# Kernel tuning notes

Hardware: AMD Instinct MI355X
Metric: run time of the kernel (lower is better)

Reference implementation:

```python
import jax, jax.numpy as jnp
import numpy as np

H_RENDER = 640   # hard-coded render resolution in the torch forward
W_RENDER = 640
OUT_H = 128      # self.height
OUT_W = 128      # self.width
NUM_VERTS = 778  # MANO hand mesh
NUM_FACES = 1538
BATCH = 4
BG_DEPTH = 1e10  # z-buffer background, clamped to 100 afterwards


def setup_inputs() -> dict:
    key = jax.random.key(0)
    k1, k2, k3 = jax.random.split(key, 3)
    # screen-space x,y in [0, 640), positive depth z
    xy = jax.random.uniform(k1, (BATCH, NUM_VERTS, 2), minval=0.0, maxval=640.0)
    z = jax.random.uniform(k2, (BATCH, NUM_VERTS, 1), minval=0.3, maxval=1.5)
    vertices = jnp.concatenate([xy, z], axis=-1).astype(jnp.float32)
    faces = jax.random.randint(k3, (NUM_FACES, 3), 0, NUM_VERTS)
    # right_hand=True: swap face columns 0 and 1 (winding flip), as in __init__
    faces = faces[:, jnp.array([1, 0, 2])].astype(jnp.int64)
    return {"vertices": vertices, "faces": faces}


def _edge(ax, ay, bx, by, px, py):
    # signed area of (a, b, p); standard rasterizer edge function
    return (bx - ax) * (py - ay) - (by - ay) * (px - ax)


def _rasterize(face_vertices):
    # face_vertices: [B, F, 3(vertex), 3(x,y,z)] -> z-buffer depth map [B, H, W]
    B = face_vertices.shape[0]
    ys, xs = jnp.meshgrid(
        jnp.arange(H_RENDER, dtype=jnp.float32) + 0.5,
        jnp.arange(W_RENDER, dtype=jnp.float32) + 0.5,
        indexing='ij',
    )  # pixel centers, [H, W]

    def step(zbuf, tri):
        # tri: [B, 3, 3] -> per-vertex coords broadcast to [B, 1, 1]
        x = tri[:, :, 0][:, :, None, None]
        y = tri[:, :, 1][:, :, None, None]
        z = tri[:, :, 2][:, :, None, None]
        x0, x1, x2 = x[:, 0], x[:, 1], x[:, 2]
        y0, y1, y2 = y[:, 0], y[:, 1], y[:, 2]
        z0, z1, z2 = z[:, 0], z[:, 1], z[:, 2]
        e0 = _edge(x1, y1, x2, y2, xs, ys)  # weight of v0
        e1 = _edge(x2, y2, x0, y0, xs, ys)  # weight of v1
        e2 = _edge(x0, y0, x1, y1, xs, ys)  # weight of v2
        area = _edge(x0, y0, x1, y1, x2, y2)  # [B,1,1]
        s = jnp.sign(area)
        valid = jnp.abs(area) > 1e-12
        inside = (e0 * s >= 0) & (e1 * s >= 0) & (e2 * s >= 0) & valid
        safe_area = jnp.where(valid, area, 1.0)
        zpix = (e0 * z0 + e1 * z1 + e2 * z2) / safe_area  # barycentric depth
        cand = jnp.where(inside, zpix, jnp.float32(BG_DEPTH))
        return jnp.minimum(zbuf, cand), None

    zbuf0 = jnp.full((B, H_RENDER, W_RENDER), BG_DEPTH, dtype=jnp.float32)
    zbuf, _ = jax.lax.scan(step, zbuf0, jnp.swapaxes(face_vertices, 0, 1))
    return zbuf


def reference(vertices, faces):
    B = vertices.shape[0]
    F = faces.shape[0]
    # vertex gather: vertices[:, faces.view(-1), 0:3].view(B, F, 3, 3)
    fv = vertices[:, faces.reshape(-1), 0:3].reshape(B, F, 3, 3)
    dm = _rasterize(fv)
    dm = jnp.minimum(dm, 100.0)  # torch.clamp(max=100.0)
    # bilinear resize, align_corners=False (half-pixel), no antialias, like F.interpolate
    resized = jax.image.resize(dm[:, None], (B, 1, OUT_H, OUT_W), method='linear', antialias=False)
    return resized[:, 0]
```

## Files before the change

### kernel.cpp

```cpp
#include <hip/hip_runtime.h>


#pragma clang fp contract(off)

#define H_OUT 128
#define W_OUT 128
#define NV 778
#define NF 1538
#define NB 4
#define NCHUNK 25
#define NFP (NCHUNK * 64)
#define BG100 0x42C80000u


__global__ __launch_bounds__(256) void prep_kernel(
    const float* __restrict__ verts,
    const int* __restrict__ faces,
    float* __restrict__ bbox,
    float* __restrict__ data,
    unsigned int* __restrict__ outu)
{
    int t = blockIdx.x * 256 + threadIdx.x;
    outu[t] = BG100;
    if (t >= NB * NFP) return;
    int b = t / NFP;
    int f = t - b * NFP;
    float* bb = bbox + (size_t)t * 4;
    if (f >= NF) {
        bb[0] = 1e30f; bb[1] = -1e30f; bb[2] = 1e30f; bb[3] = -1e30f;
        return;
    }
    int i0 = faces[f * 3 + 0];
    int i1 = faces[f * 3 + 1];
    int i2 = faces[f * 3 + 2];
    const float* vb = verts + (size_t)b * NV * 3;
    float x0 = vb[i0 * 3 + 0], y0 = vb[i0 * 3 + 1], z0 = vb[i0 * 3 + 2];
    float x1 = vb[i1 * 3 + 0], y1 = vb[i1 * 3 + 1], z1 = vb[i1 * 3 + 2];
    float x2 = vb[i2 * 3 + 0], y2 = vb[i2 * 3 + 1], z2 = vb[i2 * 3 + 2];

    float dx12 = x2 - x1, dy12 = y2 - y1;
    float dx02 = x0 - x2, dy02 = y0 - y2;
    float dx01 = x1 - x0, dy01 = y1 - y0;
    float y20 = y2 - y0, x20 = x2 - x0;
    float area = dx01 * y20 - dy01 * x20;

    float s = 0.0f;
    if (fabsf(area) > 1e-12f) s = (area > 0.0f) ? 1.0f : -1.0f;

    float xmin = fminf(fminf(x0, x1), x2), xmax = fmaxf(fmaxf(x0, x1), x2);
    float ymin = fminf(fminf(y0, y1), y2), ymax = fmaxf(fmaxf(y0, y1), y2);
    if (s == 0.0f) { xmin = 1e30f; xmax = -1e30f; }

    bb[0] = xmin; bb[1] = xmax; bb[2] = ymin; bb[3] = ymax;

    float* o = data + (size_t)t * 16;
    o[0] = s * dx12; o[1] = s * dy12;
    o[2] = s * dx02; o[3] = s * dy02;
    o[4] = s * dx01; o[5] = s * dy01;
    o[6] = x0;  o[7] = y0;  o[8] = x1;  o[9] = y1;  o[10] = x2; o[11] = y2;
    o[12] = z0; o[13] = z1; o[14] = z2; o[15] = s * area;
}

__global__ __launch_bounds__(128) void raster_kernel(
    const float* __restrict__ bbox,
    const float* __restrict__ data,
    unsigned int* __restrict__ outu)
{
    __shared__ float lds[64 * 16];

    int blk = blockIdx.x;
    int tile  = blk & 127;
    int b     = (blk >> 7) & 3;
    int chunk = blk >> 9;
    int tid = threadIdx.x;

    int gbase = b * NFP + chunk * 64;
    const float4* src = (const float4*)&data[(size_t)gbase * 16];
    ((float4*)lds)[tid]       = src[tid];
    ((float4*)lds)[tid + 128] = src[tid + 128];
    __syncthreads();

    int lane = tid & 63;
    int w = __builtin_amdgcn_readfirstlane(tid >> 6);

    int tx = tile & 7, ty = tile >> 3;
    int i = ty * 8 + w * 4 + (lane >> 4);
    int j = tx * 16 + (lane & 15);
    float px = 5.0f * (float)j + 2.5f;
    float py = 5.0f * (float)i + 2.5f;

    float px_lo = 80.0f * (float)tx + 2.5f, px_hi = px_lo + 75.0f;
    float py_lo = 40.0f * (float)ty + 20.0f * (float)w + 2.5f;
    float py_hi = py_lo + 15.0f;

    float4 bb = *(const float4*)&bbox[(size_t)(gbase + lane) * 4];
    bool ov = !(bb.x > px_hi || bb.y < px_lo || bb.z > py_hi || bb.w < py_lo);
    unsigned long long mask = __ballot(ov);

    float nb = 1e10f, ab = 1.0f;
    while (mask) {
        int f0 = __builtin_ctzll(mask); mask &= mask - 1;
        int f1 = mask ? __builtin_ctzll(mask) : f0;
        mask &= mask - 1;

        const float4* p0 = (const float4*)&lds[f0 * 16];
        const float4* p1 = (const float4*)&lds[f1 * 16];
        float4 A0 = p0[0], B0 = p0[1], C0 = p0[2], D0 = p0[3];
        float4 A1 = p1[0], B1 = p1[1], C1 = p1[2], D1 = p1[3];

        float e0 = A0.x * (py - C0.y) - A0.y * (px - C0.x);
        float e1 = A0.z * (py - C0.w) - A0.w * (px - C0.z);
        float e2 = B0.x * (py - B0.w) - B0.y * (px - B0.z);
        bool in0 = (e0 >= 0.0f) & (e1 >= 0.0f) & (e2 >= 0.0f);
        float n0 = ((e0 * D0.x) + (e1 * D0.y)) + (e2 * D0.z);
        bool t0 = in0 & (n0 * ab < nb * D0.w);
        nb = t0 ? n0 : nb;  ab = t0 ? D0.w : ab;

        float g0 = A1.x * (py - C1.y) - A1.y * (px - C1.x);
        float g1 = A1.z * (py - C1.w) - A1.w * (px - C1.z);
        float g2 = B1.x * (py - B1.w) - B1.y * (px - B1.z);
        bool in1 = (g0 >= 0.0f) & (g1 >= 0.0f) & (g2 >= 0.0f);
        float n1 = ((g0 * D1.x) + (g1 * D1.y)) + (g2 * D1.z);
        bool t1 = in1 & (n1 * ab < nb * D1.w);
        nb = t1 ? n1 : nb;  ab = t1 ? D1.w : ab;
    }

    float z = nb / ab;
    z += 0.0f;
    if (z < 1e9f)
        atomicMin(&outu[(size_t)b * (H_OUT * W_OUT) + i * W_OUT + j],
                  __float_as_uint(fminf(z, 100.0f)));
}

extern "C" void kernel_launch(void* const* d_in, const int* in_sizes, int n_in,
                              void* d_out, int out_size, void* d_ws, size_t ws_size,
                              hipStream_t stream) {
    const float* verts = (const float*)d_in[0];
    const int*   faces = (const int*)d_in[1];
    float* out = (float*)d_out;
    float* bbox = (float*)d_ws;
    float* data = bbox + (size_t)NB * NFP * 4;

    prep_kernel<<<256, 256, 0, stream>>>(verts, faces, bbox, data,
                                         (unsigned int*)out);
    raster_kernel<<<NCHUNK * NB * 128, 128, 0, stream>>>(
        bbox, data, (unsigned int*)out);
}
```

Before: 97.40 us.

## Process five face chunks per block with double-buffered LDS and final min-reduce kernel

```diff
diff --git a/kernel.cpp b/kernel.cpp
--- a/kernel.cpp
+++ b/kernel.cpp
@@ -8,20 +8,17 @@
 #define NV 778
 #define NF 1538
 #define NB 4
-#define NCHUNK 25
-#define NFP (NCHUNK * 64)
-#define BG100 0x42C80000u
+#define NFP 1600
+#define NGRP 5
 
 
 __global__ __launch_bounds__(256) void prep_kernel(
     const float* __restrict__ verts,
     const int* __restrict__ faces,
     float* __restrict__ bbox,
-    float* __restrict__ data,
-    unsigned int* __restrict__ outu)
+    float* __restrict__ data)
 {
     int t = blockIdx.x * 256 + threadIdx.x;
-    outu[t] = BG100;
     if (t >= NB * NFP) return;
     int b = t / NFP;
     int f = t - b * NFP;
@@ -64,22 +61,15 @@
 __global__ __launch_bounds__(128) void raster_kernel(
     const float* __restrict__ bbox,
     const float* __restrict__ data,
-    unsigned int* __restrict__ outu)
+    float* __restrict__ part)
 {
-    __shared__ float lds[64 * 16];
+    __shared__ float lds[2][64 * 16];
 
     int blk = blockIdx.x;
-    int tile  = blk & 127;
-    int b     = (blk >> 7) & 3;
-    int chunk = blk >> 9;
-    int tid = threadIdx.x;
-
-    int gbase = b * NFP + chunk * 64;
-    const float4* src = (const float4*)&data[(size_t)gbase * 16];
-    ((float4*)lds)[tid]       = src[tid];
-    ((float4*)lds)[tid + 128] = src[tid + 128];
-    __syncthreads();
-
+    int tile = blk & 127;
+    int b    = (blk >> 7) & 3;
+    int g    = blk >> 9;
+    int tid  = threadIdx.x;
     int lane = tid & 63;
     int w = __builtin_amdgcn_readfirstlane(tid >> 6);
 
@@ -93,43 +83,76 @@
     float py_lo = 40.0f * (float)ty + 20.0f * (float)w + 2.5f;
     float py_hi = py_lo + 15.0f;
 
-    float4 bb = *(const float4*)&bbox[(size_t)(gbase + lane) * 4];
-    bool ov = !(bb.x > px_hi || bb.y < px_lo || bb.z > py_hi || bb.w < py_lo);
-    unsigned long long mask = __ballot(ov);
+    int gbase = b * NFP + g * (5 * 64);
+    const float4* src = (const float4*)&data[(size_t)gbase * 16];
+
+    float4 d0a = src[tid], d0b = src[tid + 128];
+    float4 bb0 = *(const float4*)&bbox[(size_t)(gbase + lane) * 4];
 
     float nb = 1e10f, ab = 1.0f;
-    while (mask) {
-        int f0 = __builtin_ctzll(mask); mask &= mask - 1;
-        int f1 = mask ? __builtin_ctzll(mask) : f0;
-        mask &= mask - 1;
+    #pragma unroll
+    for (int c = 0; c < 5; ++c) {
+        float4 d1a = {}, d1b = {}, bb1 = {};
+        if (c < 4) {
+            const float4* s2 = src + (c + 1) * 256;
+            d1a = s2[tid]; d1b = s2[tid + 128];
+            bb1 = *(const float4*)&bbox[(size_t)(gbase + (c + 1) * 64 + lane) * 4];
+        }
 
-        const float4* p0 = (const float4*)&lds[f0 * 16];
-        const float4* p1 = (const float4*)&lds[f1 * 16];
-        float4 A0 = p0[0], B0 = p0[1], C0 = p0[2], D0 = p0[3];
-        float4 A1 = p1[0], B1 = p1[1], C1 = p1[2], D1 = p1[3];
+        float* L = lds[c & 1];
+        ((float4*)L)[tid]       = d0a;
+        ((float4*)L)[tid + 128] = d0b;
+        __syncthreads();
 
-        float e0 = A0.x * (py - C0.y) - A0.y * (px - C0.x);
-        float e1 = A0.z * (py - C0.w) - A0.w * (px - C0.z);
-        float e2 = B0.x * (py - B0.w) - B0.y * (px - B0.z);
-        bool in0 = (e0 >= 0.0f) & (e1 >= 0.0f) & (e2 >= 0.0f);
-        float n0 = ((e0 * D0.x) + (e1 * D0.y)) + (e2 * D0.z);
-        bool t0 = in0 & (n0 * ab < nb * D0.w);
-        nb = t0 ? n0 : nb;  ab = t0 ? D0.w : ab;
+        bool ov = !(bb0.x > px_hi || bb0.y < px_lo ||
+                    bb0.z > py_hi || bb0.w < py_lo);
+        unsigned long long mask = __ballot(ov);
 
-        float g0 = A1.x * (py - C1.y) - A1.y * (px - C1.x);
-        float g1 = A1.z * (py - C1.w) - A1.w * (px - C1.z);
-        float g2 = B1.x * (py - B1.w) - B1.y * (px - B1.z);
-        bool in1 = (g0 >= 0.0f) & (g1 >= 0.0f) & (g2 >= 0.0f);
-        float n1 = ((g0 * D1.x) + (g1 * D1.y)) + (g2 * D1.z);
-        bool t1 = in1 & (n1 * ab < nb * D1.w);
-        nb = t1 ? n1 : nb;  ab = t1 ? D1.w : ab;
+        while (mask) {
+            int f0 = __builtin_ctzll(mask); mask &= mask - 1;
+            int f1 = mask ? __builtin_ctzll(mask) : f0;
+            mask &= mask - 1;
+
+            const float4* p0 = (const float4*)&L[f0 * 16];
+            const float4* p1 = (const float4*)&L[f1 * 16];
+            float4 A0 = p0[0], B0 = p0[1], C0 = p0[2], D0 = p0[3];
+            float4 A1 = p1[0], B1 = p1[1], C1 = p1[2], D1 = p1[3];
+
+            float e0 = A0.x * (py - C0.y) - A0.y * (px - C0.x);
+            float e1 = A0.z * (py - C0.w) - A0.w * (px - C0.z);
+            float e2 = B0.x * (py - B0.w) - B0.y * (px - B0.z);
+            bool in0 = (e0 >= 0.0f) & (e1 >= 0.0f) & (e2 >= 0.0f);
+            float n0 = ((e0 * D0.x) + (e1 * D0.y)) + (e2 * D0.z);
+            bool t0 = in0 & (n0 * ab < nb * D0.w);
+            nb = t0 ? n0 : nb;  ab = t0 ? D0.w : ab;
+
+            float g0 = A1.x * (py - C1.y) - A1.y * (px - C1.x);
+            float g1 = A1.z * (py - C1.w) - A1.w * (px - C1.z);
+            float g2 = B1.x * (py - B1.w) - B1.y * (px - B1.z);
+            bool in1 = (g0 >= 0.0f) & (g1 >= 0.0f) & (g2 >= 0.0f);
+            float n1 = ((g0 * D1.x) + (g1 * D1.y)) + (g2 * D1.z);
+            bool t1 = in1 & (n1 * ab < nb * D1.w);
+            nb = t1 ? n1 : nb;  ab = t1 ? D1.w : ab;
+        }
+
+        d0a = d1a; d0b = d1b; bb0 = bb1;
     }
 
     float z = nb / ab;
-    z += 0.0f;
-    if (z < 1e9f)
-        atomicMin(&outu[(size_t)b * (H_OUT * W_OUT) + i * W_OUT + j],
-                  __float_as_uint(fminf(z, 100.0f)));
+    part[((size_t)g << 16) + ((size_t)b << 14) + (i << 7) + j] = z;
+}
+
+__global__ __launch_bounds__(256) void final_kernel(
+    const float* __restrict__ part,
+    float* __restrict__ out)
+{
+    int t = blockIdx.x * 256 + threadIdx.x;
+    float m = part[t];
+    m = fminf(m, part[t + 1 * 65536]);
+    m = fminf(m, part[t + 2 * 65536]);
+    m = fminf(m, part[t + 3 * 65536]);
+    m = fminf(m, part[t + 4 * 65536]);
+    out[t] = fminf(m, 100.0f);
 }
 
 extern "C" void kernel_launch(void* const* d_in, const int* in_sizes, int n_in,
@@ -140,9 +163,10 @@
     float* out = (float*)d_out;
     float* bbox = (float*)d_ws;
     float* data = bbox + (size_t)NB * NFP * 4;
+    float* part = data + (size_t)NB * NFP * 16;
 
-    prep_kernel<<<256, 256, 0, stream>>>(verts, faces, bbox, data,
-                                         (unsigned int*)out);
-    raster_kernel<<<NCHUNK * NB * 128, 128, 0, stream>>>(
-        bbox, data, (unsigned int*)out);
+    prep_kernel<<<(NB * NFP + 255) / 256, 256, 0, stream>>>(verts, faces,
+                                                            bbox, data);
+    raster_kernel<<<NGRP * NB * 128, 128, 0, stream>>>(bbox, data, part);
+    final_kernel<<<256, 256, 0, stream>>>(part, out);
 }
```

Result: slower. 115.8 us (+18.9%).
